# Kernel optimization log

Hardware: AMD Instinct MI355X
Metric: run time of the kernel (lower is better)

## Reference

```python
import jax, jax.numpy as jnp
import numpy as np

B, S, D, V, H = 2048, 64, 128, 256, 4
d = D // H
NB = 2        # num sLSTM blocks
NEG = -1e30   # -inf surrogate for initial stabilizer state m


def _ln(x, w, eps=1e-5):
    mu = jnp.mean(x, axis=-1, keepdims=True)
    var = jnp.var(x, axis=-1, keepdims=True)
    return (x - mu) * jax.lax.rsqrt(var + eps) * w


def _headnorm(y, w, eps=1e-5):
    # y: [B,S,H,d]; normalize per head over d, learnable scale over full D
    mu = jnp.mean(y, axis=-1, keepdims=True)
    var = jnp.var(y, axis=-1, keepdims=True)
    yn = (y - mu) * jax.lax.rsqrt(var + eps)
    return yn.reshape(y.shape[0], y.shape[1], D) * w


def _slstm(x, Wg, R, b):
    # x:[B,S,D]  Wg:[4,H,d,d] per-head gate projections  R:[H,d,4,d] recurrent  b:[4,D]
    xh = x.reshape(x.shape[0], x.shape[1], H, d)
    # gate preactivations from input, precomputed for all timesteps: [S,B,4,H,d]
    Wx = jnp.einsum('bshd,ghde->sbghe', xh, Wg) + b.reshape(1, 1, 4, H, d)

    def step(carry, wx_t):
        y, c, n, m = carry  # each [B,H,d]
        raw = wx_t + jnp.einsum('bhd,hdge->bghe', y, R)  # [B,4,H,d]
        iraw, fraw, zraw, oraw = raw[:, 0], raw[:, 1], raw[:, 2], raw[:, 3]
        logfplusm = m + jax.nn.log_sigmoid(fraw)
        mnew = jnp.maximum(iraw, logfplusm)           # stabilizer
        igate = jnp.exp(iraw - mnew)
        fgate = jnp.exp(logfplusm - mnew)
        cnew = fgate * c + igate * jnp.tanh(zraw)
        nnew = fgate * n + igate
        ynew = jax.nn.sigmoid(oraw) * cnew / nnew
        return (ynew, cnew, nnew, mnew), ynew

    zero = jnp.zeros((x.shape[0], H, d), x.dtype)
    m0 = jnp.full((x.shape[0], H, d), NEG, x.dtype)
    _, ys = jax.lax.scan(step, (zero, zero, zero, m0), Wx)
    return jnp.moveaxis(ys, 0, 1)  # [B,S,H,d]


def setup_inputs():
    key = jax.random.key(0)
    ks = jax.random.split(key, 8)
    g = lambda k, shp, sc: jax.random.normal(k, shp, jnp.float32) * sc
    return {
        'x': jax.random.randint(ks[0], (B, S), 0, V),
        'embed': g(ks[1], (V, D), 0.02),
        'Wg': g(ks[2], (NB, 4, H, d, d), d ** -0.5),
        'R': g(ks[3], (NB, H, d, 4, d), d ** -0.5),
        'b': g(ks[4], (NB, 4, D), 0.02),
        'ln1_w': jnp.ones((NB, D), jnp.float32),
        'gn_w': jnp.ones((NB, D), jnp.float32),
        'ln2_w': jnp.ones((NB, D), jnp.float32),
        'W_up': g(ks[5], (NB, D, 2 * D), D ** -0.5),
        'W_down': g(ks[6], (NB, D, D), D ** -0.5),
        'post_w': jnp.ones((D,), jnp.float32),
        'proj_W': g(ks[7], (D, V), D ** -0.5),
        'proj_b': jnp.zeros((V,), jnp.float32),
    }


def reference(x, embed, Wg, R, b, ln1_w, gn_w, ln2_w, W_up, W_down, post_w, proj_W, proj_b):
    h = embed[x]  # [B,S,D]
    for l in range(NB):
        # pre-norm sLSTM sublayer with residual
        y = _slstm(_ln(h, ln1_w[l]), Wg[l], R[l], b[l])
        h = h + _headnorm(y, gn_w[l])
        # pre-norm gated FFN (proj_factor=1.0, gelu gate) with residual
        z = _ln(h, ln2_w[l])
        up = z @ W_up[l]
        h = h + (jax.nn.gelu(up[..., :D], approximate=False) * up[..., D:]) @ W_down[l]
    return _ln(h, post_w) @ proj_W + proj_b  # [B,S,V]
```

## Files before the change

### kernel.cpp

```cpp
#include <hip/hip_runtime.h>
#include <stdint.h>
#include <math.h>

#define BB 2048
#define SS 64
#define DD 128
#define HH 4
#define DH 32
#define VV 256
#define NTOK (BB*SS)

typedef short v8s __attribute__((ext_vector_type(8)));
typedef float v4f __attribute__((ext_vector_type(4)));

__device__ __forceinline__ float bf2f(unsigned short u){
  union { unsigned int i; float f; } v; v.i = ((unsigned int)u) << 16; return v.f;
}
__device__ __forceinline__ unsigned short f2bf(float f){
  union { unsigned int i; float f; } v; v.f = f;
  unsigned int r = v.i + 0x7FFFu + ((v.i >> 16) & 1u);
  return (unsigned short)(r >> 16);
}

__device__ __forceinline__ float fexp2(float x){ return __builtin_amdgcn_exp2f(x); }
__device__ __forceinline__ float flog2(float x){ return __builtin_amdgcn_logf(x); }
__device__ __forceinline__ float frcp (float x){ return __builtin_amdgcn_rcpf(x); }
__device__ __forceinline__ float frsq (float x){ return __builtin_amdgcn_rsqf(x); }

#define L2E 1.44269504088896340736f

#define O_EMB 0
#define O_WG  32768
#define O_R   65536
#define O_BG  98304
#define O_LN1 99328
#define O_GN  99584
#define O_LN2 99840
#define O_WUP 100096
#define O_WDN 165632
#define O_PW  198400
#define O_PWT 198528
#define O_PB  231296
#define O_TOT 231552

__global__ void k_prep(const void* s0, const void* s1, const void* s2, const void* s3,
                       const void* s4, const void* s5, const void* s6, const void* s7,
                       const void* s8, const void* s9, const void* s10, const void* s11,
                       const unsigned int* sniff, unsigned short* dst)
{
  bool f32 = (*sniff == 0x3F800000u);
  int i = blockIdx.x * 256 + threadIdx.x;
  if (i >= O_TOT) return;
  int base;
  const void* src;
  if      (i < O_WG ){ base=O_EMB; src=s0; }
  else if (i < O_R  ){ base=O_WG;  src=s1; }
  else if (i < O_BG ){ base=O_R;   src=s2; }
  else if (i < O_LN1){ base=O_BG;  src=s3; }
  else if (i < O_GN ){ base=O_LN1; src=s4; }
  else if (i < O_LN2){ base=O_GN;  src=s5; }
  else if (i < O_WUP){ base=O_LN2; src=s6; }
  else if (i < O_WDN){ base=O_WUP; src=s7; }
  else if (i < O_PW ){ base=O_WDN; src=s8; }
  else if (i < O_PWT){ base=O_PW;  src=s9; }
  else if (i < O_PB ){ base=O_PWT; src=s10; }
  else               { base=O_PB;  src=s11; }
  int j = i - base;
  dst[i] = f32 ? f2bf(((const float*)src)[j]) : ((const unsigned short*)src)[j];
}

__global__ void k_embed_ln(const int* __restrict__ x, const unsigned short* __restrict__ emb,
                           const unsigned short* __restrict__ w,
                           float* __restrict__ h, unsigned short* __restrict__ o){
  int row  = blockIdx.x * 4 + (threadIdx.x >> 6);
  int lane = threadIdx.x & 63;
  int c = lane * 2;
  unsigned int ev = *(const unsigned int*)(emb + (size_t)x[row] * DD + c);
  float x0 = bf2f((unsigned short)(ev & 0xFFFF));
  float x1 = bf2f((unsigned short)(ev >> 16));
  float* hp = h + (size_t)row * DD + c;
  hp[0] = x0; hp[1] = x1;
  float s1 = x0 + x1, s2 = x0*x0 + x1*x1;
  #pragma unroll
  for (int m = 1; m < 64; m <<= 1){ s1 += __shfl_xor(s1, m, 64); s2 += __shfl_xor(s2, m, 64); }
  float mu  = s1 * (1.f/128.f);
  float var = fmaxf(s2 * (1.f/128.f) - mu*mu, 0.f);
  float rs  = rsqrtf(var + 1e-5f);
  unsigned int o0 = f2bf((x0 - mu) * rs * bf2f(w[c]));
  unsigned int o1 = f2bf((x1 - mu) * rs * bf2f(w[c+1]));
  *(unsigned int*)(o + (size_t)row * DD + c) = o0 | (o1 << 16);
}

__launch_bounds__(256, 1)
__global__ void k_rec(unsigned short* xy,
                      const unsigned short* __restrict__ Wg, const unsigned short* __restrict__ R,
                      const unsigned short* __restrict__ bgate)
{
  __shared__ __align__(16) unsigned short ysh[HH][8][DH];
  int tid = threadIdx.x;
  int wv = tid >> 6;
  int lane = tid & 63;
  int quad = lane >> 4, l16 = lane & 15;
  int b0 = blockIdx.x * 8;

  for (int i = lane; i < 8*DH; i += 64) ((unsigned short*)&ysh[wv][0][0])[i] = 0;

  v8s wgf[8], rf[8];
  float bias[8];
  #pragma unroll
  for (int nt = 0; nt < 8; nt++){
    int c = nt*16 + l16;
    int g = c >> 5, e = c & 31;
    v8s a, r8;
    #pragma unroll
    for (int j = 0; j < 8; j++){
      int k = quad*8 + j;
      a[j]  = (short)Wg[((size_t)(g*HH + wv)*DH + k)*DH + e];
      r8[j] = (short)R [((size_t)(wv*DH + k)*4 + g)*DH + e];
    }
    wgf[nt] = a; rf[nt] = r8;
    bias[nt] = bf2f(bgate[g*DD + wv*DH + e]);
  }

  int ehl  = quad >> 1;
  int rq   = quad & 1;
  int ecol = ehl*16 + l16;

  float cst[4], nst[4], m2[4];
  #pragma unroll
  for (int i = 0; i < 4; i++){ cst[i] = 0.f; nst[i] = 0.f; m2[i] = -1e30f; }

  int m = l16 & 7;
  const unsigned short* xbase = xy + ((size_t)(b0 + m) * SS) * DD + wv*DH + quad*8;
  unsigned short* ybase = xy + ((size_t)b0 * SS) * DD + wv*DH + ecol;

  v8s ax = *(const v8s*)xbase;
  for (int s = 0; s < SS; s++){
    v8s axn;
    if (s < SS-1) axn = *(const v8s*)(xbase + (size_t)(s+1) * DD);
    v8s ay = *(const v8s*)&ysh[wv][m][quad*8];

    v4f acc[8];
    #pragma unroll
    for (int nt = 0; nt < 8; nt++){
      v4f a; a[0] = bias[nt]; a[1] = bias[nt]; a[2] = bias[nt]; a[3] = bias[nt];
      a = __builtin_amdgcn_mfma_f32_16x16x32_bf16(ay, rf[nt],  a, 0, 0, 0);
      a = __builtin_amdgcn_mfma_f32_16x16x32_bf16(ax, wgf[nt], a, 0, 0, 0);
      acc[nt] = a;
    }

    v4f ai4 = ehl ? acc[1] : acc[0];
    v4f af4 = ehl ? acc[3] : acc[2];
    v4f az4 = ehl ? acc[5] : acc[4];
    v4f ao4 = ehl ? acc[7] : acc[6];

    #pragma unroll
    for (int r = 0; r < 4; r++){
      float iv2 = ai4[r] * L2E;
      float fl2 = -flog2(1.f + fexp2(-L2E * af4[r]));
      float lpm = m2[r] + fl2;
      float mn  = fmaxf(iv2, lpm);
      float ig  = fexp2(iv2 - mn);
      float fg  = fexp2(lpm - mn);
      float ez  = fexp2((2.f*L2E) * az4[r]);
      float tz  = 1.f - 2.f * frcp(1.f + ez);
      float cn  = fg * cst[r] + ig * tz;
      float nn  = fg * nst[r] + ig;
      cst[r] = cn; nst[r] = nn; m2[r] = mn;
      float eo  = fexp2(-L2E * ao4[r]);
      unsigned short yb = f2bf(cn * frcp(nn * (1.f + eo)));
      ybase[((size_t)((rq*4 + r) * SS + s)) * DD] = yb;
      ysh[wv][rq*4 + r][ecol] = yb;
    }
    ax = axn;
  }
}

__launch_bounds__(256)
__global__ void k_ffn(float* __restrict__ h, unsigned short* yz,
                      const unsigned short* __restrict__ Wup, const unsigned short* __restrict__ Wdn,
                      const unsigned short* __restrict__ gnw, const unsigned short* __restrict__ znw,
                      const unsigned short* __restrict__ lnw, int write_h)
{
  __shared__ __align__(16) unsigned short Zt[16][DD];
  __shared__ __align__(16) unsigned short G[16][DD];
  __shared__ __align__(16) float Hv[16][DD+4];
  __shared__ float P[4][16][2];
  int tid = threadIdx.x, wv = tid >> 6, lane = tid & 63, quad = lane >> 4, l16 = lane & 15;

  v8s bu[4][4];
  #pragma unroll
  for (int ni = 0; ni < 4; ni++){
    int nt = (ni < 2) ? (2*wv + ni) : (2*wv + 8 + (ni - 2));
    int col = nt*16 + l16;
    #pragma unroll
    for (int ks = 0; ks < 4; ks++){
      v8s t;
      #pragma unroll
      for (int j = 0; j < 8; j++){ int k = ks*32 + quad*8 + j; t[j] = (short)Wup[(size_t)k*256 + col]; }
      bu[ni][ks] = t;
    }
  }
  v8s bd[2][4];
  #pragma unroll
  for (int ni = 0; ni < 2; ni++){
    int col = (2*wv + ni)*16 + l16;
    #pragma unroll
    for (int ks = 0; ks < 4; ks++){
      v8s t;
      #pragma unroll
      for (int j = 0; j < 8; j++){ int k = ks*32 + quad*8 + j; t[j] = (short)Wdn[(size_t)k*DD + col]; }
      bd[ni][ks] = t;
    }
  }
  float lw0 = bf2f(lnw[(2*wv+0)*16 + l16]);
  float lw1 = bf2f(lnw[(2*wv+1)*16 + l16]);

  int prow = wv*4 + quad;
  int c0 = l16 * 8;
  float gw[8], zw[8];
  #pragma unroll
  for (int j = 0; j < 8; j++){ gw[j] = bf2f(gnw[c0+j]); zw[j] = bf2f(znw[c0+j]); }

  for (int tt = 0; tt < 8; tt++){
    int tok0 = (blockIdx.x * 8 + tt) * 16;

    v8s yv = *(const v8s*)(yz + (size_t)(tok0 + prow) * DD + c0);
    v4f ha = *(const v4f*)(h + (size_t)(tok0 + prow) * DD + c0);
    v4f hb = *(const v4f*)(h + (size_t)(tok0 + prow) * DD + c0 + 4);
    float yf[8];
    #pragma unroll
    for (int j = 0; j < 8; j++) yf[j] = bf2f((unsigned short)yv[j]);
    float p1 = 0.f, p2 = 0.f;
    #pragma unroll
    for (int j = 0; j < 8; j++){ p1 += yf[j]; p2 += yf[j]*yf[j]; }
    p1 += __shfl_xor(p1, 1, 64); p2 += __shfl_xor(p2, 1, 64);
    p1 += __shfl_xor(p1, 2, 64); p2 += __shfl_xor(p2, 2, 64);
    float hmu = p1 * (1.f/32.f);
    float hvr = fmaxf(p2 * (1.f/32.f) - hmu*hmu, 0.f);
    float hrs = frsq(hvr + 1e-5f);
    float hv[8];
    #pragma unroll
    for (int j = 0; j < 8; j++){
      float hval = (j < 4) ? ha[j] : hb[j-4];
      hv[j] = hval + (yf[j] - hmu) * hrs * gw[j];
    }
    float s1 = 0.f, s2 = 0.f;
    #pragma unroll
    for (int j = 0; j < 8; j++){ s1 += hv[j]; s2 += hv[j]*hv[j]; }
    #pragma unroll
    for (int mk = 1; mk < 16; mk <<= 1){ s1 += __shfl_xor(s1, mk, 64); s2 += __shfl_xor(s2, mk, 64); }
    float mu  = s1 * (1.f/128.f);
    float var = fmaxf(s2 * (1.f/128.f) - mu*mu, 0.f);
    float rs  = frsq(var + 1e-5f);
    *(v4f*)&Hv[prow][c0]     = v4f{hv[0], hv[1], hv[2], hv[3]};
    *(v4f*)&Hv[prow][c0 + 4] = v4f{hv[4], hv[5], hv[6], hv[7]};
    v8s zb;
    #pragma unroll
    for (int j = 0; j < 8; j++) zb[j] = (short)f2bf((hv[j] - mu) * rs * zw[j]);
    *(v8s*)&Zt[prow][(l16 ^ (prow & 7)) * 8] = zb;
    __syncthreads();

    v8s az[4];
    #pragma unroll
    for (int ks = 0; ks < 4; ks++)
      az[ks] = *(const v8s*)&Zt[l16][((ks*4 + quad) ^ (l16 & 7)) * 8];
    v4f acc[4];
    #pragma unroll
    for (int ni = 0; ni < 4; ni++){
      v4f a = {0.f, 0.f, 0.f, 0.f};
      #pragma unroll
      for (int ks = 0; ks < 4; ks++) a = __builtin_amdgcn_mfma_f32_16x16x32_bf16(az[ks], bu[ni][ks], a, 0, 0, 0);
      acc[ni] = a;
    }
    #pragma unroll
    for (int i = 0; i < 2; i++){
      int colc = (2*wv + i)*2 + (l16 >> 3);
      #pragma unroll
      for (int r = 0; r < 4; r++){
        float u1 = acc[i][r], u2 = acc[2+i][r];
        float gv = 0.5f * u1 * (1.f + erff(u1 * 0.70710678118654752f)) * u2;
        int grow = quad*4 + r;
        G[grow][((colc ^ (grow & 7)) << 3) + (l16 & 7)] = f2bf(gv);
      }
    }
    __syncthreads();
    v8s ag[4];
    #pragma unroll
    for (int ks = 0; ks < 4; ks++)
      ag[ks] = *(const v8s*)&G[l16][((ks*4 + quad) ^ (l16 & 7)) * 8];
    v4f o2[2];
    #pragma unroll
    for (int ni = 0; ni < 2; ni++){
      v4f a = {0.f, 0.f, 0.f, 0.f};
      #pragma unroll
      for (int ks = 0; ks < 4; ks++) a = __builtin_amdgcn_mfma_f32_16x16x32_bf16(ag[ks], bd[ni][ks], a, 0, 0, 0);
      o2[ni] = a;
    }

    float hn[2][4];
    #pragma unroll
    for (int r = 0; r < 4; r++){
      #pragma unroll
      for (int ni = 0; ni < 2; ni++){
        int row = quad*4 + r, col = (2*wv + ni)*16 + l16;
        float v = Hv[row][col] + o2[ni][r];
        if (write_h) h[((size_t)(tok0 + row)) * DD + col] = v;
        hn[ni][r] = v;
      }
      float a1 = hn[0][r] + hn[1][r];
      float a2 = hn[0][r]*hn[0][r] + hn[1][r]*hn[1][r];
      #pragma unroll
      for (int mk = 1; mk < 16; mk <<= 1){ a1 += __shfl_xor(a1, mk, 64); a2 += __shfl_xor(a2, mk, 64); }
      if (l16 == 0){ P[wv][quad*4 + r][0] = a1; P[wv][quad*4 + r][1] = a2; }
    }
    __syncthreads();
    #pragma unroll
    for (int r = 0; r < 4; r++){
      int row = quad*4 + r;
      float S1 = P[0][row][0] + P[1][row][0] + P[2][row][0] + P[3][row][0];
      float S2 = P[0][row][1] + P[1][row][1] + P[2][row][1] + P[3][row][1];
      float mu2  = S1 * (1.f/128.f);
      float var2 = fmaxf(S2 * (1.f/128.f) - mu2*mu2, 0.f);
      float rs2  = rsqrtf(var2 + 1e-5f);
      size_t rb = ((size_t)(tok0 + row)) * DD;
      yz[rb + (2*wv+0)*16 + l16] = f2bf((hn[0][r] - mu2) * rs2 * lw0);
      yz[rb + (2*wv+1)*16 + l16] = f2bf((hn[1][r] - mu2) * rs2 * lw1);
    }
    __syncthreads();
  }
}

__launch_bounds__(256)
__global__ void k_proj(const unsigned short* __restrict__ z, const unsigned short* __restrict__ W,
                       const unsigned short* __restrict__ pb, float* __restrict__ out)
{
  int tid = threadIdx.x, wv = tid >> 6, lane = tid & 63, quad = lane >> 4, l16 = lane & 15;
  v8s bw[4][4];
  float bias[4];
  #pragma unroll
  for (int ni = 0; ni < 4; ni++){
    int col = (4*wv + ni)*16 + l16;
    bias[ni] = bf2f(pb[col]);
    #pragma unroll
    for (int ks = 0; ks < 4; ks++){
      v8s t;
      #pragma unroll
      for (int j = 0; j < 8; j++){ int k = ks*32 + quad*8 + j; t[j] = (short)W[(size_t)k*VV + col]; }
      bw[ni][ks] = t;
    }
  }
  for (int tt = 0; tt < 8; tt++){
    int tok0 = (blockIdx.x * 8 + tt) * 16;
    v8s az[4];
    #pragma unroll
    for (int ks = 0; ks < 4; ks++)
      az[ks] = *(const v8s*)(z + ((size_t)(tok0 + l16)) * DD + ks*32 + quad*8);
    #pragma unroll
    for (int ni = 0; ni < 4; ni++){
      v4f a = {0.f, 0.f, 0.f, 0.f};
      #pragma unroll
      for (int ks = 0; ks < 4; ks++) a = __builtin_amdgcn_mfma_f32_16x16x32_bf16(az[ks], bw[ni][ks], a, 0, 0, 0);
      int col = (4*wv + ni)*16 + l16;
      #pragma unroll
      for (int r = 0; r < 4; r++)
        out[((size_t)(tok0 + quad*4 + r)) * VV + col] = a[r] + bias[ni];
    }
  }
}

extern "C" void kernel_launch(void* const* d_in, const int* in_sizes, int n_in,
                              void* d_out, int out_size, void* d_ws, size_t ws_size,
                              hipStream_t stream)
{
  const int* x = (const int*)d_in[0];
  float* out = (float*)d_out;

  float* h = (float*)d_ws;
  unsigned short* xnb = (unsigned short*)(h + (size_t)NTOK * DD);
  unsigned short* wts = xnb + (size_t)NTOK * DD;

  k_prep<<<(O_TOT + 255)/256, 256, 0, stream>>>(
      d_in[1], d_in[2], d_in[3], d_in[4], d_in[5], d_in[6], d_in[7],
      d_in[8], d_in[9], d_in[10], d_in[11], d_in[12],
      (const unsigned int*)d_in[5], wts);

  const unsigned short* emb = wts + O_EMB;
  const unsigned short* Wg  = wts + O_WG;
  const unsigned short* R   = wts + O_R;
  const unsigned short* bg  = wts + O_BG;
  const unsigned short* ln1 = wts + O_LN1;
  const unsigned short* gn  = wts + O_GN;
  const unsigned short* ln2 = wts + O_LN2;
  const unsigned short* Wup = wts + O_WUP;
  const unsigned short* Wdn = wts + O_WDN;
  const unsigned short* pw  = wts + O_PW;
  const unsigned short* pW  = wts + O_PWT;
  const unsigned short* pbv = wts + O_PB;

  k_embed_ln<<<NTOK/4, 256, 0, stream>>>(x, emb, ln1, h, xnb);
  for (int l = 0; l < 2; l++){
    k_rec <<<256, 256, 0, stream>>>(xnb, Wg + l*16384, R + l*16384, bg + l*512);
    const unsigned short* nextln = (l == 0) ? (ln1 + DD) : pw;
    k_ffn <<<1024, 256, 0, stream>>>(h, xnb, Wup + l*32768, Wdn + l*16384,
                                     gn + l*DD, ln2 + l*DD, nextln, (l == 0) ? 1 : 0);
  }
  k_proj<<<1024, 256, 0, stream>>>(xnb, pW, pbv, out);
}
```

Measured before the change: 431.9 us.

## Split sLSTM recurrence into 2-sequence blocks for more parallelism

The recurrent kernel now gives each block 2 batch sequences instead of 8, which launches 1024 blocks instead of 256. The launch bound asks for 4 blocks per CU. Each lane now carries one (row, column) state instead of four, which shortens the serial per-step elementwise chain and raises occupancy so the latency of the sequential scan can be hidden. In exchange, most MFMA rows do wasted work (16-row tiles with only 2 real rows), and each block reloads the full weight fragments into registers.

```diff
diff --git a/kernel.cpp b/kernel.cpp
--- a/kernel.cpp
+++ b/kernel.cpp
@@ -91,19 +91,19 @@
   *(unsigned int*)(o + (size_t)row * DD + c) = o0 | (o1 << 16);
 }
 
-__launch_bounds__(256, 1)
+__launch_bounds__(256, 4)
 __global__ void k_rec(unsigned short* xy,
                       const unsigned short* __restrict__ Wg, const unsigned short* __restrict__ R,
                       const unsigned short* __restrict__ bgate)
 {
-  __shared__ __align__(16) unsigned short ysh[HH][8][DH];
+  __shared__ __align__(16) unsigned short ysh[HH][2][DH];
   int tid = threadIdx.x;
   int wv = tid >> 6;
   int lane = tid & 63;
   int quad = lane >> 4, l16 = lane & 15;
-  int b0 = blockIdx.x * 8;
-
-  for (int i = lane; i < 8*DH; i += 64) ((unsigned short*)&ysh[wv][0][0])[i] = 0;
+  int b0 = blockIdx.x * 2;
+
+  for (int i = lane; i < 2*DH; i += 64) ((unsigned short*)&ysh[wv][0][0])[i] = 0;
 
   v8s wgf[8], rf[8];
   float bias[8];
@@ -122,17 +122,15 @@
     bias[nt] = bf2f(bgate[g*DD + wv*DH + e]);
   }
 
-  int ehl  = quad >> 1;
-  int rq   = quad & 1;
-  int ecol = ehl*16 + l16;
-
-  float cst[4], nst[4], m2[4];
-  #pragma unroll
-  for (int i = 0; i < 4; i++){ cst[i] = 0.f; nst[i] = 0.f; m2[i] = -1e30f; }
-
-  int m = l16 & 7;
+  int rb   = quad & 1;
+  int colh = quad >> 1;
+  int col  = colh*16 + l16;
+
+  float cst = 0.f, nst = 0.f, m2 = -1e30f;
+
+  int m = l16 & 1;
   const unsigned short* xbase = xy + ((size_t)(b0 + m) * SS) * DD + wv*DH + quad*8;
-  unsigned short* ybase = xy + ((size_t)b0 * SS) * DD + wv*DH + ecol;
+  unsigned short* ybase = xy + ((size_t)(b0 + rb) * SS) * DD + wv*DH + col;
 
   v8s ax = *(const v8s*)xbase;
   for (int s = 0; s < SS; s++){
@@ -149,29 +147,30 @@
       acc[nt] = a;
     }
 
-    v4f ai4 = ehl ? acc[1] : acc[0];
-    v4f af4 = ehl ? acc[3] : acc[2];
-    v4f az4 = ehl ? acc[5] : acc[4];
-    v4f ao4 = ehl ? acc[7] : acc[6];
-
-    #pragma unroll
-    for (int r = 0; r < 4; r++){
-      float iv2 = ai4[r] * L2E;
-      float fl2 = -flog2(1.f + fexp2(-L2E * af4[r]));
-      float lpm = m2[r] + fl2;
-      float mn  = fmaxf(iv2, lpm);
-      float ig  = fexp2(iv2 - mn);
-      float fg  = fexp2(lpm - mn);
-      float ez  = fexp2((2.f*L2E) * az4[r]);
-      float tz  = 1.f - 2.f * frcp(1.f + ez);
-      float cn  = fg * cst[r] + ig * tz;
-      float nn  = fg * nst[r] + ig;
-      cst[r] = cn; nst[r] = nn; m2[r] = mn;
-      float eo  = fexp2(-L2E * ao4[r]);
-      unsigned short yb = f2bf(cn * frcp(nn * (1.f + eo)));
-      ybase[((size_t)((rq*4 + r) * SS + s)) * DD] = yb;
-      ysh[wv][rq*4 + r][ecol] = yb;
-    }
+    v4f ai4 = colh ? acc[1] : acc[0];
+    v4f af4 = colh ? acc[3] : acc[2];
+    v4f az4 = colh ? acc[5] : acc[4];
+    v4f ao4 = colh ? acc[7] : acc[6];
+    float iv = rb ? ai4[1] : ai4[0];
+    float fv = rb ? af4[1] : af4[0];
+    float zv = rb ? az4[1] : az4[0];
+    float ov = rb ? ao4[1] : ao4[0];
+
+    float iv2 = iv * L2E;
+    float fl2 = -flog2(1.f + fexp2(-L2E * fv));
+    float lpm = m2 + fl2;
+    float mn  = fmaxf(iv2, lpm);
+    float ig  = fexp2(iv2 - mn);
+    float fg  = fexp2(lpm - mn);
+    float ez  = fexp2((2.f*L2E) * zv);
+    float tz  = 1.f - 2.f * frcp(1.f + ez);
+    float cn  = fg * cst + ig * tz;
+    float nn  = fg * nst + ig;
+    cst = cn; nst = nn; m2 = mn;
+    float eo  = fexp2(-L2E * ov);
+    unsigned short yb = f2bf(cn * frcp(nn * (1.f + eo)));
+    ysh[wv][rb][col] = yb;
+    ybase[(size_t)s * DD] = yb;
     ax = axn;
   }
 }
@@ -400,7 +399,7 @@
 
   k_embed_ln<<<NTOK/4, 256, 0, stream>>>(x, emb, ln1, h, xnb);
   for (int l = 0; l < 2; l++){
-    k_rec <<<256, 256, 0, stream>>>(xnb, Wg + l*16384, R + l*16384, bg + l*512);
+    k_rec <<<BB/2, 256, 0, stream>>>(xnb, Wg + l*16384, R + l*16384, bg + l*512);
     const unsigned short* nextln = (l == 0) ? (ln1 + DD) : pw;
     k_ffn <<<1024, 256, 0, stream>>>(h, xnb, Wup + l*32768, Wdn + l*16384,
                                      gn + l*DD, ln2 + l*DD, nextln, (l == 0) ? 1 : 0);
```

After: 524.3 us. 1.21x slower.
